# Performance work log

Measured on AMD Instinct MI355X. Metric: run time of the kernel, lower is better.

The kernel has to match this reference:

```python
import jax, jax.numpy as jnp
import numpy as np

E = 256
H = 8
DK = E // H


def setup_inputs() -> dict:
    key = jax.random.key(0)
    ks = jax.random.split(key, 16)
    B, NA, NB = 2, 2048, 2048
    x_a = jax.random.normal(ks[0], (B, NA, E), dtype=jnp.float32)
    x_b = jax.random.normal(ks[1], (B, NB, E), dtype=jnp.float32)
    s = 1.0 / np.sqrt(E)  # kaiming-normal-ish scale
    inp = {"x_a": x_a, "x_b": x_b}
    names = ["wq", "wk_a", "wk_b", "wv_a", "wv_b", "w"]
    for i, n in enumerate(names):
        inp[n + "_w"] = jax.random.normal(ks[2 + 2 * i], (E, E), dtype=jnp.float32) * s
        inp[n + "_b"] = jax.random.normal(ks[3 + 2 * i], (E,), dtype=jnp.float32) * 0.01
    return inp


def _linear(x, w, b):
    # torch nn.Linear: y = x @ w.T + b
    return jnp.einsum('bne,fe->bnf', x, w) + b


def _heads(x):
    # [B, N, E] -> [B, H, N, DK]
    B, N, _ = x.shape
    return x.reshape(B, N, H, DK).transpose(0, 2, 1, 3)


def reference(x_a, x_b, wq_w, wq_b, wk_a_w, wk_a_b, wk_b_w, wk_b_b,
              wv_a_w, wv_a_b, wv_b_w, wv_b_b, w_w, w_b):
    B, NA, _ = x_a.shape
    q = _heads(_linear(x_a, wq_w, wq_b))          # [B,H,NA,DK]
    k_a = _heads(_linear(x_a, wk_a_w, wk_a_b))    # [B,H,NA,DK]
    v_a = _heads(_linear(x_a, wv_a_w, wv_a_b))
    k_b = _heads(_linear(x_b, wk_b_w, wk_b_b))    # [B,H,NB,DK]
    v_b = _heads(_linear(x_b, wv_b_w, wv_b_b))
    k = jnp.concatenate([k_a, k_b], axis=2)       # [B,H,NA+NB,DK]
    v = jnp.concatenate([v_a, v_b], axis=2)
    scores = jnp.einsum('bhqd,bhkd->bhqk', q, k) / jnp.sqrt(jnp.float32(DK))
    p = jax.nn.softmax(scores, axis=-1)           # [B,H,NA,NA+NB]
    z = jnp.einsum('bhqk,bhkd->bhqd', p, v)       # [B,H,NA,DK]
    z = z.transpose(0, 2, 1, 3).reshape(B, NA, E)
    out = _linear(z, w_w, w_b) + x_a
    return out
```

## Files before the change

### kernel.cpp

```cpp
#include <hip/hip_runtime.h>
#include <cstdint>

typedef short bf16x8 __attribute__((ext_vector_type(8)));
typedef float f32x4 __attribute__((ext_vector_type(4)));
typedef unsigned short u16;
typedef unsigned int u32;

#define DEVI static __device__ __forceinline__


DEVI u16 f2bf(float f) {
  u32 x = __builtin_bit_cast(u32, f);
  x += 0x7fffu + ((x >> 16) & 1u);
  return (u16)(x >> 16);
}

DEVI u32 pack_bf2(float lo, float hi) {
  return (u32)f2bf(lo) | ((u32)f2bf(hi) << 16);
}

DEVI u32 cvt_pk_bf16(float lo, float hi) {
  u32 r;
  asm("v_cvt_pk_bf16_f32 %0, %1, %2" : "=v"(r) : "v"(lo), "v"(hi));
  return r;
}

DEVI f32x4 mfma16(bf16x8 a, bf16x8 b, f32x4 c) {
  return __builtin_amdgcn_mfma_f32_16x16x32_bf16(a, b, c, 0, 0, 0);
}

DEVI void load_lds16(const void* g, void* l) {
  __builtin_amdgcn_global_load_lds(
      (const __attribute__((address_space(1))) u32*)g,
      (__attribute__((address_space(3))) u32*)l, 16, 0, 0);
}

#define CSCALE 0.2550351f

DEVI int rho(int k) {
  return ((k >> 5) << 5) | (((k >> 2) & 1) << 4) | (((k >> 3) & 3) << 2) | (k & 3);
}

__global__ __launch_bounds__(256) void convert_kernel(
    const float* __restrict__ xa, const float* __restrict__ xb,
    const float* __restrict__ w0, const float* __restrict__ w1,
    const float* __restrict__ w2, const float* __restrict__ w3,
    const float* __restrict__ w4, const float* __restrict__ w5,
    u16* __restrict__ dst) {
  int i = (int)(blockIdx.x * 256u + threadIdx.x) * 8;
  const float* s;
  if (i < 1048576) {
    s = xa + i;
  } else if (i < 2097152) {
    s = xb + (i - 1048576);
  } else {
    int t = i - 2097152;
    int j = t >> 16, o = t & 65535;
    s = (j == 0 ? w0 : j == 1 ? w1 : j == 2 ? w2 : j == 3 ? w3 : j == 4 ? w4 : w5) + o;
  }
  float4 a = *(const float4*)s;
  float4 b = *(const float4*)(s + 4);
  uint4 o4;
  o4.x = pack_bf2(a.x, a.y);
  o4.y = pack_bf2(a.z, a.w);
  o4.z = pack_bf2(b.x, b.y);
  o4.w = pack_bf2(b.z, b.w);
  *(uint4*)(dst + i) = o4;
}

__global__ __launch_bounds__(256) void proj_kernel(
    const u16* __restrict__ xa_bf, const u16* __restrict__ xb_bf,
    const u16* __restrict__ wbase,
    const float* __restrict__ b0, const float* __restrict__ b1,
    const float* __restrict__ b2, const float* __restrict__ b3,
    const float* __restrict__ b4,
    u16* __restrict__ Qo, u16* __restrict__ Ko, u16* __restrict__ Vo) {
  int job = blockIdx.z;
  const u16* A = (job <= 2) ? xa_bf : xb_bf;
  const u16* W = wbase + job * 65536;
  const float* bias = job == 0 ? b0 : job == 1 ? b1 : job == 2 ? b2 : job == 3 ? b3 : b4;
  int mode = (job == 0) ? 0 : (job == 1 || job == 3) ? 1 : 2;
  int soff = (job >= 3) ? 2048 : 0;

  int tid = threadIdx.x, wid = tid >> 6, lane = tid & 63, g = lane >> 4, c = lane & 15;
  int m0 = blockIdx.x * 64, n0 = blockIdx.y * 64;
  const u16* Ap = A + (m0 + wid * 16 + c) * 256 + g * 8;
  const u16* Wp = W + (n0 + c) * 256 + g * 8;
  f32x4 acc[4] = {};
#pragma unroll
  for (int kk = 0; kk < 256; kk += 32) {
    bf16x8 af = *(const bf16x8*)(Ap + kk);
#pragma unroll
    for (int nt = 0; nt < 4; ++nt) {
      bf16x8 bfr = *(const bf16x8*)(Wp + nt * 4096 + kk);
      acc[nt] = mfma16(af, bfr, acc[nt]);
    }
  }
#pragma unroll
  for (int nt = 0; nt < 4; ++nt) {
    int f = n0 + nt * 16 + c;
    float bv = bias[f];
    int h = f >> 5, d = f & 31;
#pragma unroll
    for (int r = 0; r < 4; ++r) {
      int m = m0 + wid * 16 + g * 4 + r;
      int bq = m >> 11, n = m & 2047;
      int bh = bq * 8 + h;
      float y = acc[nt][r] + bv;
      if (mode == 0) {
        Qo[(bh * 2048 + n) * 32 + d] = f2bf(y * CSCALE);
      } else if (mode == 1) {
        int nk = soff + n;
        int pr = (nk & ~63) | rho(nk & 63);
        Ko[((size_t)bh * 4096 + pr) * 32 + d] = f2bf(y);
      } else {
        int nk = soff + n;
        Vo[(size_t)bh * 131072 + (nk >> 6) * 2048 + ((nk >> 3) & 7) * 256 +
           d * 8 + (nk & 7)] = f2bf(y);
      }
    }
  }
}

__global__ __launch_bounds__(256) void attn_kernel(
    const u16* __restrict__ Q, const u16* __restrict__ K,
    const u16* __restrict__ Vt, float* __restrict__ Zp, float* __restrict__ S) {
  __shared__ __align__(16) unsigned char sbuf[24576];
  int bid = blockIdx.x;
  int xcd = bid & 7, slot = bid >> 3;
  int bh = (xcd << 1) | (slot & 1);
  int rem = slot >> 1;
  int ks = rem & 1, qi = rem >> 1;
  int tid = threadIdx.x, wid = tid >> 6, lane = tid & 63;
  int g = lane >> 4, c = lane & 15;
  int qbase = qi * 64 + wid * 16;

  const unsigned char* Kb =
      (const unsigned char*)K + ((size_t)bh * 4096 + ks * 2048) * 64;
  const unsigned char* Vb =
      (const unsigned char*)Vt + (size_t)bh * 262144 + (size_t)ks * 131072;

  bf16x8 qf = *(const bf16x8*)(Q + ((size_t)bh * 2048 + qbase + c) * 32 + g * 8);

  int kaddr = c * 64 + ((g ^ ((c >> 1) & 3)) << 4);
  int vaddr = g * 512 + c * 16;

  int o = wid * 1024 + (lane << 4);
  int ko_src = o ^ (((o >> 7) & 3) << 4);

  f32x4 z0 = {}, z1 = {};
  float lsum = 0.f;

  load_lds16(Kb + ko_src, sbuf + wid * 1024);
  load_lds16(Vb + o, sbuf + 12288 + wid * 1024);

  int cur = 0;
  for (int t = 0; t < 32; ++t) {
    int nxt = cur + 1;
    if (nxt == 3) nxt = 0;
    if (t + 1 < 32) {
      load_lds16(Kb + (t + 1) * 4096 + ko_src, sbuf + nxt * 4096 + wid * 1024);
      load_lds16(Vb + (t + 1) * 4096 + o, sbuf + 12288 + nxt * 4096 + wid * 1024);
      __builtin_amdgcn_sched_barrier(0);
      asm volatile("s_waitcnt vmcnt(2)" ::: "memory");
    } else {
      __builtin_amdgcn_sched_barrier(0);
      asm volatile("s_waitcnt vmcnt(0)" ::: "memory");
    }
    __builtin_amdgcn_s_barrier();
    __builtin_amdgcn_sched_barrier(0);

    const unsigned char* kbuf = sbuf + cur * 4096;
    const unsigned char* vbuf = sbuf + 12288 + cur * 4096;

    bf16x8 kf0 = *(const bf16x8*)(kbuf + kaddr);
    bf16x8 kf1 = *(const bf16x8*)(kbuf + kaddr + 1024);
    bf16x8 kf2 = *(const bf16x8*)(kbuf + kaddr + 2048);
    bf16x8 kf3 = *(const bf16x8*)(kbuf + kaddr + 3072);
    bf16x8 vf00 = *(const bf16x8*)(vbuf + vaddr);
    bf16x8 vf01 = *(const bf16x8*)(vbuf + vaddr + 2048);
    bf16x8 vf10 = *(const bf16x8*)(vbuf + vaddr + 256);
    bf16x8 vf11 = *(const bf16x8*)(vbuf + vaddr + 2048 + 256);

    f32x4 zz = {};
    __builtin_amdgcn_s_setprio(1);
    f32x4 s0 = mfma16(kf0, qf, zz);
    f32x4 s1 = mfma16(kf1, qf, zz);
    f32x4 s2 = mfma16(kf2, qf, zz);
    f32x4 s3 = mfma16(kf3, qf, zz);
    __builtin_amdgcn_s_setprio(0);

    float e0[4], e1[4], e2[4], e3[4];
#pragma unroll
    for (int r = 0; r < 4; ++r) {
      e0[r] = __builtin_amdgcn_exp2f(s0[r]);
      e1[r] = __builtin_amdgcn_exp2f(s1[r]);
      e2[r] = __builtin_amdgcn_exp2f(s2[r]);
      e3[r] = __builtin_amdgcn_exp2f(s3[r]);
    }
    lsum += ((e0[0] + e0[1]) + (e0[2] + e0[3])) + ((e1[0] + e1[1]) + (e1[2] + e1[3])) +
            ((e2[0] + e2[1]) + (e2[2] + e2[3])) + ((e3[0] + e3[1]) + (e3[2] + e3[3]));

    union { u32 u[4]; bf16x8 v; } A0, A1;
    A0.u[0] = cvt_pk_bf16(e0[0], e0[1]);
    A0.u[1] = cvt_pk_bf16(e0[2], e0[3]);
    A0.u[2] = cvt_pk_bf16(e1[0], e1[1]);
    A0.u[3] = cvt_pk_bf16(e1[2], e1[3]);
    A1.u[0] = cvt_pk_bf16(e2[0], e2[1]);
    A1.u[1] = cvt_pk_bf16(e2[2], e2[3]);
    A1.u[2] = cvt_pk_bf16(e3[0], e3[1]);
    A1.u[3] = cvt_pk_bf16(e3[2], e3[3]);

    __builtin_amdgcn_s_setprio(1);
    z0 = mfma16(A0.v, vf00, z0);
    z0 = mfma16(A1.v, vf01, z0);
    z1 = mfma16(A0.v, vf10, z1);
    z1 = mfma16(A1.v, vf11, z1);
    __builtin_amdgcn_s_setprio(0);
    cur = nxt;
  }

  lsum += __shfl_xor(lsum, 16);
  lsum += __shfl_xor(lsum, 32);

  size_t zrow = ((size_t)ks * 16 + bh) * 2048;
  if (lane < 16) S[zrow + qbase + lane] = lsum;
#pragma unroll
  for (int r = 0; r < 4; ++r) {
    int m = qbase + g * 4 + r;
    float* zp = Zp + (zrow + m) * 32;
    zp[c] = z0[r];
    zp[16 + c] = z1[r];
  }
}

__global__ __launch_bounds__(256) void out_kernel(
    const float* __restrict__ Zp, const float* __restrict__ S,
    const u16* __restrict__ W, const float* __restrict__ bias,
    const float* __restrict__ resid, float* __restrict__ out) {
  int tid = threadIdx.x, wid = tid >> 6, lane = tid & 63, g = lane >> 4, c = lane & 15;
  int m0 = blockIdx.x * 16;
  int mrow = m0 + c;
  int bq = mrow >> 11, n = mrow & 2047;
  const u16* Wp = W + (wid * 64 + c) * 256 + g * 8;
  f32x4 acc[4] = {};
#pragma unroll
  for (int h = 0; h < 8; ++h) {
    int bh = bq * 8 + h;
    const float* za = Zp + ((size_t)bh * 2048 + n) * 32 + g * 8;
    const float* zb = za + (size_t)16 * 2048 * 32;
    float4 a0 = *(const float4*)za;
    float4 a1 = *(const float4*)(za + 4);
    float4 b0 = *(const float4*)zb;
    float4 b1 = *(const float4*)(zb + 4);
    float inv = 1.0f / (S[(size_t)bh * 2048 + n] + S[(size_t)(16 + bh) * 2048 + n]);
    union { u32 u[4]; bf16x8 v; } cv;
    cv.u[0] = pack_bf2((a0.x + b0.x) * inv, (a0.y + b0.y) * inv);
    cv.u[1] = pack_bf2((a0.z + b0.z) * inv, (a0.w + b0.w) * inv);
    cv.u[2] = pack_bf2((a1.x + b1.x) * inv, (a1.y + b1.y) * inv);
    cv.u[3] = pack_bf2((a1.z + b1.z) * inv, (a1.w + b1.w) * inv);
    bf16x8 af = cv.v;
#pragma unroll
    for (int nt = 0; nt < 4; ++nt) {
      bf16x8 bfr = *(const bf16x8*)(Wp + nt * 4096 + h * 32);
      acc[nt] = mfma16(af, bfr, acc[nt]);
    }
  }
#pragma unroll
  for (int nt = 0; nt < 4; ++nt) {
    int f = wid * 64 + nt * 16 + c;
    float bv = bias[f];
#pragma unroll
    for (int r = 0; r < 4; ++r) {
      int m = m0 + g * 4 + r;
      out[(size_t)m * 256 + f] = acc[nt][r] + bv + resid[(size_t)m * 256 + f];
    }
  }
}

extern "C" void kernel_launch(void* const* d_in, const int* in_sizes, int n_in,
                              void* d_out, int out_size, void* d_ws, size_t ws_size,
                              hipStream_t stream) {
  const float* xa = (const float*)d_in[0];
  const float* xb = (const float*)d_in[1];
  const float* wq_w = (const float*)d_in[2];
  const float* wq_b = (const float*)d_in[3];
  const float* wka_w = (const float*)d_in[4];
  const float* wka_b = (const float*)d_in[5];
  const float* wkb_w = (const float*)d_in[6];
  const float* wkb_b = (const float*)d_in[7];
  const float* wva_w = (const float*)d_in[8];
  const float* wva_b = (const float*)d_in[9];
  const float* wvb_w = (const float*)d_in[10];
  const float* wvb_b = (const float*)d_in[11];
  const float* w_w = (const float*)d_in[12];
  const float* w_b = (const float*)d_in[13];

  u16* ws = (u16*)d_ws;
  u16* xa_bf = ws;
  u16* xb_bf = ws + 1048576;
  u16* wbf = ws + 2097152;
  u16* Qb = ws + 2490368;
  u16* Kb = ws + 3538944;
  u16* Vtb = ws + 5636096;
  float* Zp = (float*)(ws + 7733248);
  float* S = (float*)((char*)d_ws + 23855104);

  convert_kernel<<<1216, 256, 0, stream>>>(xa, xb, wq_w, wka_w, wva_w, wkb_w,
                                           wvb_w, w_w, ws);
  proj_kernel<<<dim3(64, 4, 5), 256, 0, stream>>>(
      xa_bf, xb_bf, wbf, wq_b, wka_b, wva_b, wkb_b, wvb_b, Qb, Kb, Vtb);
  attn_kernel<<<1024, 256, 0, stream>>>(Qb, Kb, Vtb, Zp, S);
  out_kernel<<<256, 256, 0, stream>>>(Zp, S, wbf + 5 * 65536, w_b, xa,
                                      (float*)d_out);
}
```

Baseline: 78.35 us.

## Split attention keys into four chunks and combine partials in output projection

Measured after the change: 80.68 us. 1.03x slower.

```diff
diff --git a/kernel.cpp b/kernel.cpp
--- a/kernel.cpp
+++ b/kernel.cpp
@@ -84,7 +84,7 @@
 
   int tid = threadIdx.x, wid = tid >> 6, lane = tid & 63, g = lane >> 4, c = lane & 15;
   int m0 = blockIdx.x * 64, n0 = blockIdx.y * 64;
-  const u16* Ap = A + (m0 + wid * 16 + c) * 256 + g * 8;
+  const u16* Ap = A + (size_t)(m0 + wid * 16 + c) * 256 + g * 8;
   const u16* Wp = W + (n0 + c) * 256 + g * 8;
   f32x4 acc[4] = {};
 #pragma unroll
@@ -108,7 +108,7 @@
       int bh = bq * 8 + h;
       float y = acc[nt][r] + bv;
       if (mode == 0) {
-        Qo[(bh * 2048 + n) * 32 + d] = f2bf(y * CSCALE);
+        Qo[((size_t)bh * 2048 + n) * 32 + d] = f2bf(y * CSCALE);
       } else if (mode == 1) {
         int nk = soff + n;
         int pr = (nk & ~63) | rho(nk & 63);
@@ -130,15 +130,15 @@
   int xcd = bid & 7, slot = bid >> 3;
   int bh = (xcd << 1) | (slot & 1);
   int rem = slot >> 1;
-  int ks = rem & 1, qi = rem >> 1;
+  int ks = rem & 3, qi = rem >> 2;
   int tid = threadIdx.x, wid = tid >> 6, lane = tid & 63;
   int g = lane >> 4, c = lane & 15;
   int qbase = qi * 64 + wid * 16;
 
   const unsigned char* Kb =
-      (const unsigned char*)K + ((size_t)bh * 4096 + ks * 2048) * 64;
+      (const unsigned char*)K + (size_t)bh * 262144 + (size_t)ks * 65536;
   const unsigned char* Vb =
-      (const unsigned char*)Vt + (size_t)bh * 262144 + (size_t)ks * 131072;
+      (const unsigned char*)Vt + (size_t)bh * 262144 + (size_t)ks * 65536;
 
   bf16x8 qf = *(const bf16x8*)(Q + ((size_t)bh * 2048 + qbase + c) * 32 + g * 8);
 
@@ -155,10 +155,10 @@
   load_lds16(Vb + o, sbuf + 12288 + wid * 1024);
 
   int cur = 0;
-  for (int t = 0; t < 32; ++t) {
+  for (int t = 0; t < 16; ++t) {
     int nxt = cur + 1;
     if (nxt == 3) nxt = 0;
-    if (t + 1 < 32) {
+    if (t + 1 < 16) {
       load_lds16(Kb + (t + 1) * 4096 + ko_src, sbuf + nxt * 4096 + wid * 1024);
       load_lds16(Vb + (t + 1) * 4096 + o, sbuf + 12288 + nxt * 4096 + wid * 1024);
       __builtin_amdgcn_sched_barrier(0);
@@ -242,28 +242,41 @@
   int m0 = blockIdx.x * 16;
   int mrow = m0 + c;
   int bq = mrow >> 11, n = mrow & 2047;
-  const u16* Wp = W + (wid * 64 + c) * 256 + g * 8;
+  const u16* Wp = W + (size_t)(wid * 64 + c) * 256 + g * 8;
+
   f32x4 acc[4] = {};
 #pragma unroll
   for (int h = 0; h < 8; ++h) {
     int bh = bq * 8 + h;
-    const float* za = Zp + ((size_t)bh * 2048 + n) * 32 + g * 8;
-    const float* zb = za + (size_t)16 * 2048 * 32;
-    float4 a0 = *(const float4*)za;
-    float4 a1 = *(const float4*)(za + 4);
-    float4 b0 = *(const float4*)zb;
-    float4 b1 = *(const float4*)(zb + 4);
-    float inv = 1.0f / (S[(size_t)bh * 2048 + n] + S[(size_t)(16 + bh) * 2048 + n]);
-    union { u32 u[4]; bf16x8 v; } cv;
-    cv.u[0] = pack_bf2((a0.x + b0.x) * inv, (a0.y + b0.y) * inv);
-    cv.u[1] = pack_bf2((a0.z + b0.z) * inv, (a0.w + b0.w) * inv);
-    cv.u[2] = pack_bf2((a1.x + b1.x) * inv, (a1.y + b1.y) * inv);
-    cv.u[3] = pack_bf2((a1.z + b1.z) * inv, (a1.w + b1.w) * inv);
-    bf16x8 af = cv.v;
+    size_t sb = (size_t)bh * 2048 + n;
+    float ts = (S[sb] + S[sb + 32768]) + (S[sb + 65536] + S[sb + 98304]);
+    float iv = 1.0f / ts;
+    const float* zp = Zp + sb * 32 + g * 8;
+    float4 a0 = *(const float4*)zp;
+    float4 a1 = *(const float4*)(zp + 4);
+    float4 b0 = *(const float4*)(zp + 1048576);
+    float4 b1 = *(const float4*)(zp + 1048576 + 4);
+    float4 c0 = *(const float4*)(zp + 2097152);
+    float4 c1 = *(const float4*)(zp + 2097152 + 4);
+    float4 d0 = *(const float4*)(zp + 3145728);
+    float4 d1 = *(const float4*)(zp + 3145728 + 4);
+    float e0 = ((a0.x + b0.x) + (c0.x + d0.x)) * iv;
+    float e1 = ((a0.y + b0.y) + (c0.y + d0.y)) * iv;
+    float e2 = ((a0.z + b0.z) + (c0.z + d0.z)) * iv;
+    float e3 = ((a0.w + b0.w) + (c0.w + d0.w)) * iv;
+    float e4 = ((a1.x + b1.x) + (c1.x + d1.x)) * iv;
+    float e5 = ((a1.y + b1.y) + (c1.y + d1.y)) * iv;
+    float e6 = ((a1.z + b1.z) + (c1.z + d1.z)) * iv;
+    float e7 = ((a1.w + b1.w) + (c1.w + d1.w)) * iv;
+    union { u32 u[4]; bf16x8 v; } af;
+    af.u[0] = cvt_pk_bf16(e0, e1);
+    af.u[1] = cvt_pk_bf16(e2, e3);
+    af.u[2] = cvt_pk_bf16(e4, e5);
+    af.u[3] = cvt_pk_bf16(e6, e7);
 #pragma unroll
     for (int nt = 0; nt < 4; ++nt) {
       bf16x8 bfr = *(const bf16x8*)(Wp + nt * 4096 + h * 32);
-      acc[nt] = mfma16(af, bfr, acc[nt]);
+      acc[nt] = mfma16(af.v, bfr, acc[nt]);
     }
   }
 #pragma unroll
@@ -304,13 +317,13 @@
   u16* Kb = ws + 3538944;
   u16* Vtb = ws + 5636096;
   float* Zp = (float*)(ws + 7733248);
-  float* S = (float*)((char*)d_ws + 23855104);
+  float* S = Zp + 4194304;
 
   convert_kernel<<<1216, 256, 0, stream>>>(xa, xb, wq_w, wka_w, wva_w, wkb_w,
                                            wvb_w, w_w, ws);
   proj_kernel<<<dim3(64, 4, 5), 256, 0, stream>>>(
       xa_bf, xb_bf, wbf, wq_b, wka_b, wva_b, wkb_b, wvb_b, Qb, Kb, Vtb);
-  attn_kernel<<<1024, 256, 0, stream>>>(Qb, Kb, Vtb, Zp, S);
+  attn_kernel<<<2048, 256, 0, stream>>>(Qb, Kb, Vtb, Zp, S);
   out_kernel<<<256, 256, 0, stream>>>(Zp, S, wbf + 5 * 65536, w_b, xa,
                                       (float*)d_out);
 }
```
